# Kernel tuning notes

Hardware: AMD Instinct MI355X
Metric: run time of the kernel (lower is better)

## Reference

```python
import jax, jax.numpy as jnp
import numpy as np

N_NODES = 100000
N_EDGES = 1000000
C_IN, C_HID, C_OUT = 128, 64, 32


def _gcn_layer(x, W, b, src, dst, n):
    """PyG GCNConv with default add_self_loops=True, symmetric normalization.

    x: [N, in], W: [in, out], b: [out], src/dst: [E] int
    """
    h = x @ W  # [N, out] -- transform before aggregation
    # degree of each node counting the added self loop
    deg = jax.ops.segment_sum(jnp.ones_like(dst, dtype=h.dtype), dst, num_segments=n) + 1.0
    dinv = jax.lax.rsqrt(deg)  # deg >= 1 so always finite
    norm = dinv[src] * dinv[dst]  # [E]
    msg = h[src] * norm[:, None]  # [E, out]
    agg = jax.ops.segment_sum(msg, dst, num_segments=n)  # [N, out]
    # self-loop contribution: norm_ii = dinv_i * dinv_i
    out = agg + h * (dinv * dinv)[:, None]
    return out + b


def setup_inputs() -> dict:
    key = jax.random.key(0)
    k1, k2, k3, k4 = jax.random.split(key, 4)
    x = jax.random.normal(k1, (N_NODES, C_IN), dtype=jnp.float32)
    edge_index = jax.random.randint(k2, (2, N_EDGES), 0, N_NODES, dtype=jnp.int64)
    # Glorot-style init for the two GCN layers
    W1 = jax.random.normal(k3, (C_IN, C_HID), dtype=jnp.float32) / np.sqrt(C_IN)
    b1 = jnp.zeros((C_HID,), dtype=jnp.float32)
    W2 = jax.random.normal(k4, (C_HID, C_OUT), dtype=jnp.float32) / np.sqrt(C_HID)
    b2 = jnp.zeros((C_OUT,), dtype=jnp.float32)
    return {"x": x, "edge_index": edge_index, "W1": W1, "b1": b1, "W2": W2, "b2": b2}


def reference(x, edge_index, W1, b1, W2, b2):
    src, dst = edge_index[0], edge_index[1]
    n = x.shape[0]
    h = _gcn_layer(x, W1, b1, src, dst, n)
    h = jax.nn.relu(h)  # Dropout(0.1) is identity in eval mode
    out = _gcn_layer(h, W2, b2, src, dst, n)
    return out
```

## Files before the change

kernel.cpp:

```cpp
#include <hip/hip_runtime.h>
#include <hip/hip_fp16.h>

#define N_NODES 100000
#define N_EDGES 1000000
#define C_IN 128
#define C_HID 64
#define C_OUT 32
#define NB1 ((N_NODES + 255) / 256)
#define GT_BLOCKS 1563
#define RG_RANK_BLOCKS 781
#define RG_GRID 2344
#define AGG1_BLOCKS 6250

__global__ __launch_bounds__(256) void k_rg1(const unsigned int* __restrict__ ei,
                                             int* __restrict__ deg,
                                             int* __restrict__ rank,
                                             const float* __restrict__ x,
                                             const float* __restrict__ W1,
                                             __half* __restrict__ hs1h) {
    __shared__ float xt[64 * C_IN];
    const int bid = blockIdx.x;
    const int m = bid % 3;
    const int r = bid / 3;

    if (m == 2) {
        const bool is64 = __all(ei[2 * (threadIdx.x & 63) + 1] == 0u);
        const int T = RG_RANK_BLOCKS * 256;
        const int t = r * 256 + threadIdx.x;
        int d[6];
#pragma unroll
        for (int i = 0; i < 6; ++i) {
            int e = t + i * T;
            if (e < N_EDGES)
                d[i] = is64 ? ((const int2*)ei)[(size_t)N_EDGES + e].x
                            : (int)ei[(size_t)N_EDGES + e];
        }
        int rk[6];
#pragma unroll
        for (int i = 0; i < 6; ++i) {
            int e = t + i * T;
            if (e < N_EDGES) rk[i] = atomicAdd(&deg[d[i]], 1);
        }
#pragma unroll
        for (int i = 0; i < 6; ++i) {
            int e = t + i * T;
            if (e < N_EDGES) __builtin_nontemporal_store(rk[i], &rank[e]);
        }
        return;
    }

    const int tile = 2 * r + m;
    if (tile >= GT_BLOCKS) return;
    const int t = threadIdx.x;
    {
        const float4* x4g = (const float4*)x;
        float4* xt4w = (float4*)xt;
        const size_t base = (size_t)tile * 64 * (C_IN / 4);
        const size_t xmax = (size_t)N_NODES * (C_IN / 4) - 1;
#pragma unroll
        for (int j = 0; j < 8; ++j) {
            size_t idx = base + t + j * 256;
            if (idx > xmax) idx = xmax;
            xt4w[t + j * 256] = x4g[idx];
        }
    }
    __syncthreads();
    const int c2 = t & 31;
    const int h  = (t >> 5) & 1;
    const int wid = t >> 6;
    const int lrow0 = wid * 16 + h * 8;
    const int grow0 = tile * 64 + lrow0;
    const float4* xt4 = (const float4*)xt;

    float acc0[8] = {0, 0, 0, 0, 0, 0, 0, 0};
    float acc1[8] = {0, 0, 0, 0, 0, 0, 0, 0};
#pragma unroll 2
    for (int k4 = 0; k4 < C_IN / 4; ++k4) {
        float4 xv[8];
#pragma unroll
        for (int rr = 0; rr < 8; ++rr)
            xv[rr] = xt4[(lrow0 + rr) * (C_IN / 4) + k4];
        float2 wv[4];
#pragma unroll
        for (int j = 0; j < 4; ++j)
            wv[j] = *reinterpret_cast<const float2*>(&W1[(k4 * 4 + j) * C_HID + 2 * c2]);
#pragma unroll
        for (int rr = 0; rr < 8; ++rr) {
            acc0[rr] = fmaf(xv[rr].x, wv[0].x, acc0[rr]);
            acc1[rr] = fmaf(xv[rr].x, wv[0].y, acc1[rr]);
            acc0[rr] = fmaf(xv[rr].y, wv[1].x, acc0[rr]);
            acc1[rr] = fmaf(xv[rr].y, wv[1].y, acc1[rr]);
            acc0[rr] = fmaf(xv[rr].z, wv[2].x, acc0[rr]);
            acc1[rr] = fmaf(xv[rr].z, wv[2].y, acc1[rr]);
            acc0[rr] = fmaf(xv[rr].w, wv[3].x, acc0[rr]);
            acc1[rr] = fmaf(xv[rr].w, wv[3].y, acc1[rr]);
        }
    }
    __half2* h2o = (__half2*)hs1h;
#pragma unroll
    for (int rr = 0; rr < 8; ++rr) {
        int gr = grow0 + rr;
        if (gr < N_NODES)
            h2o[(size_t)gr * 32 + c2] = __floats2half2_rn(acc0[rr], acc1[rr]);
    }
}

__global__ __launch_bounds__(256) void k_scan1(const int* __restrict__ deg,
                                               int* __restrict__ rowstart,
                                               int* __restrict__ blksum,
                                               float* __restrict__ dinv) {
    __shared__ int sm[256];
    int i = blockIdx.x * 256 + threadIdx.x;
    int v = (i < N_NODES) ? deg[i] : 0;
    if (i < N_NODES) dinv[i] = rsqrtf((float)v + 1.0f);
    sm[threadIdx.x] = v;
    __syncthreads();
    for (int o = 1; o < 256; o <<= 1) {
        int t = (threadIdx.x >= o) ? sm[threadIdx.x - o] : 0;
        __syncthreads();
        sm[threadIdx.x] += t;
        __syncthreads();
    }
    if (i < N_NODES) rowstart[i] = sm[threadIdx.x] - v;
    if (threadIdx.x == 255) blksum[blockIdx.x] = sm[255];
}

__global__ __launch_bounds__(512) void k_scan2(const int* __restrict__ blksum,
                                               int* __restrict__ blkoff) {
    __shared__ int sm[512];
    int v = (threadIdx.x < NB1) ? blksum[threadIdx.x] : 0;
    sm[threadIdx.x] = v;
    __syncthreads();
    for (int o = 1; o < 512; o <<= 1) {
        int t = (threadIdx.x >= o) ? sm[threadIdx.x - o] : 0;
        __syncthreads();
        sm[threadIdx.x] += t;
        __syncthreads();
    }
    if (threadIdx.x < NB1) blkoff[threadIdx.x] = sm[threadIdx.x] - v;
}

__global__ __launch_bounds__(256) void k_scan3(int* __restrict__ rowstart,
                                               const int* __restrict__ blkoff) {
    int i = blockIdx.x * 256 + threadIdx.x;
    if (i < N_NODES) rowstart[i] += blkoff[i >> 8];
    if (i == 0) rowstart[N_NODES] = N_EDGES;
}

__global__ __launch_bounds__(256) void k_fill2(const unsigned int* __restrict__ ei,
                                               const int* __restrict__ rowstart,
                                               const int* __restrict__ rank,
                                               int* __restrict__ esrc) {
    const bool is64 = __all(ei[2 * (threadIdx.x & 63) + 1] == 0u);
    const int T = gridDim.x * 256;
    const int t = blockIdx.x * 256 + threadIdx.x;
#pragma unroll
    for (int i = 0; i < 4; ++i) {
        int e = t + i * T;
        if (e < N_EDGES) {
            int s, d;
            if (is64) {
                s = ((const int2*)ei)[e].x;
                d = ((const int2*)ei)[(size_t)N_EDGES + e].x;
            } else {
                s = (int)ei[e];
                d = (int)ei[(size_t)N_EDGES + e];
            }
            int p = rowstart[d] + rank[e];
            __builtin_nontemporal_store(s, &esrc[p]);
        }
    }
}

__global__ __launch_bounds__(256) void k_agg1g2(const int* __restrict__ rowstart,
                                                const int* __restrict__ esrc,
                                                const __half* __restrict__ hs1h,
                                                const float* __restrict__ dinv,
                                                const float* __restrict__ b1,
                                                const float* __restrict__ W2,
                                                __half* __restrict__ hs2h) {
    __shared__ float2 yrow[4][32];
    const int wid = threadIdx.x >> 6;
    const int lane = threadIdx.x & 63;
    const int c2 = lane & 31;
    const int eo = lane >> 5;
    float Wreg[32];
#pragma unroll
    for (int kk = 0; kk < 16; ++kk) {
        Wreg[2 * kk]     = W2[(32 * eo + 2 * kk) * C_OUT + c2];
        Wreg[2 * kk + 1] = W2[(32 * eo + 2 * kk + 1) * C_OUT + c2];
    }
    const __half2* h2 = (const __half2*)hs1h;
    const float2 bb = { b1[2 * c2], b1[2 * c2 + 1] };
    const int waveId = blockIdx.x * 4 + wid;

    for (int node = waveId; node < N_NODES; node += AGG1_BLOCKS * 4) {
        const int beg = rowstart[node], end = rowstart[node + 1];
        float2 acc; acc.x = 0.f; acc.y = 0.f;
        for (int j0 = beg; j0 < end; j0 += 16) {
            const int jj = j0 + eo;
            int idx[8];
#pragma unroll
            for (int s = 0; s < 8; ++s) {
                int j = jj + 2 * s;
                idx[s] = esrc[j < end ? j : beg];
            }
            float ds[8];
#pragma unroll
            for (int s = 0; s < 8; ++s)
                ds[s] = (jj + 2 * s < end) ? dinv[idx[s]] : 0.f;
            float2 v[8];
#pragma unroll
            for (int s = 0; s < 8; ++s)
                v[s] = __half22float2(h2[(size_t)idx[s] * 32 + c2]);
#pragma unroll
            for (int s = 0; s < 8; ++s) {
                acc.x = fmaf(ds[s], v[s].x, acc.x);
                acc.y = fmaf(ds[s], v[s].y, acc.y);
            }
        }
        acc.x += __shfl_xor(acc.x, 32);
        acc.y += __shfl_xor(acc.y, 32);
        const float dv = dinv[node];
        float2 self = __half22float2(h2[(size_t)node * 32 + c2]);
        float2 y;
        y.x = fmaxf(fmaf(dv, fmaf(dv, self.x, acc.x), bb.x), 0.f);
        y.y = fmaxf(fmaf(dv, fmaf(dv, self.y, acc.y), bb.y), 0.f);
        yrow[wid][c2] = y;
        __builtin_amdgcn_wave_barrier();
        float o = 0.f;
#pragma unroll
        for (int kk = 0; kk < 16; ++kk) {
            float2 yv = yrow[wid][16 * eo + kk];
            o = fmaf(yv.x, Wreg[2 * kk], o);
            o = fmaf(yv.y, Wreg[2 * kk + 1], o);
        }
        __builtin_amdgcn_wave_barrier();
        o += __shfl_xor(o, 32);
        if (eo == 0)
            hs2h[(size_t)node * C_OUT + c2] = __float2half(o * dv);
    }
}

__global__ __launch_bounds__(256) void k_agg2(const int* __restrict__ rowstart,
                                              const int* __restrict__ esrc,
                                              const __half* __restrict__ hs2h,
                                              const float* __restrict__ dinv,
                                              const float* __restrict__ b2,
                                              float* __restrict__ out) {
    const int node = blockIdx.x * 4 + (threadIdx.x >> 6);
    const int lane = threadIdx.x & 63;
    const int c2 = lane & 15;
    const int eo = lane >> 4;
    const __half2* h2 = (const __half2*)hs2h;
    const int beg = rowstart[node], end = rowstart[node + 1];
    float2 acc; acc.x = 0.f; acc.y = 0.f;
    for (int j0 = beg; j0 < end; j0 += 16) {
        const int jj = j0 + eo;
        int idx[4];
#pragma unroll
        for (int s = 0; s < 4; ++s) {
            int j = jj + 4 * s;
            idx[s] = esrc[j < end ? j : beg];
        }
        float2 v[4];
#pragma unroll
        for (int s = 0; s < 4; ++s)
            v[s] = __half22float2(h2[(size_t)idx[s] * 16 + c2]);
#pragma unroll
        for (int s = 0; s < 4; ++s) {
            if (jj + 4 * s < end) { acc.x += v[s].x; acc.y += v[s].y; }
        }
    }
    acc.x += __shfl_xor(acc.x, 16);
    acc.y += __shfl_xor(acc.y, 16);
    acc.x += __shfl_xor(acc.x, 32);
    acc.y += __shfl_xor(acc.y, 32);
    if (eo == 0) {
        float2 self = __half22float2(h2[(size_t)node * 16 + c2]);
        float dv = dinv[node];
        float2 o;
        o.x = fmaf(dv, acc.x + self.x, b2[2 * c2]);
        o.y = fmaf(dv, acc.y + self.y, b2[2 * c2 + 1]);
        reinterpret_cast<float2*>(out)[(size_t)node * 16 + c2] = o;
    }
}

extern "C" void kernel_launch(void* const* d_in, const int* in_sizes, int n_in,
                              void* d_out, int out_size, void* d_ws, size_t ws_size,
                              hipStream_t stream) {
    const float* x  = (const float*)d_in[0];
    const unsigned int* ei = (const unsigned int*)d_in[1];
    const float* W1 = (const float*)d_in[2];
    const float* b1 = (const float*)d_in[3];
    const float* W2 = (const float*)d_in[4];
    const float* b2 = (const float*)d_in[5];
    float* out = (float*)d_out;

    char* ws = (char*)d_ws;
    size_t off = 0;
    auto take = [&](size_t bytes) {
        char* p = ws + off;
        off += (bytes + 255) & ~(size_t)255;
        return p;
    };
    int*    esrc     = (int*)   take((size_t)N_EDGES * 4);
    int*    rank     = (int*)   take((size_t)N_EDGES * 4);
    int*    deg      = (int*)   take((size_t)N_NODES * 4);
    int*    rowstart = (int*)   take((size_t)(N_NODES + 1) * 4);
    int*    blksum   = (int*)   take((size_t)NB1 * 4);
    int*    blkoff   = (int*)   take((size_t)NB1 * 4);
    float*  dinv     = (float*) take((size_t)N_NODES * 4);
    __half* hs1h     = (__half*)take((size_t)N_NODES * C_HID * 2);
    __half* hs2h     = (__half*)take((size_t)N_NODES * C_OUT * 2);

    hipMemsetAsync(deg, 0, (size_t)N_NODES * 4, stream);
    k_rg1<<<RG_GRID, 256, 0, stream>>>(ei, deg, rank, x, W1, hs1h);

    k_scan1<<<NB1, 256, 0, stream>>>(deg, rowstart, blksum, dinv);
    k_scan2<<<1, 512, 0, stream>>>(blksum, blkoff);
    k_scan3<<<NB1, 256, 0, stream>>>(rowstart, blkoff);

    k_fill2<<<1024, 256, 0, stream>>>(ei, rowstart, rank, esrc);

    k_agg1g2<<<AGG1_BLOCKS, 256, 0, stream>>>(rowstart, esrc, hs1h, dinv, b1, W2, hs2h);

    k_agg2<<<N_NODES / 4, 256, 0, stream>>>(rowstart, esrc, hs2h, dinv, b2, out);
}
```

Baseline: 272.6 us.

## Merge scan and CSR fill into one persistent kernel with grid barriers

Replaces the three-kernel scan and the separate fill kernel with a single 196-block kernel. It uses atomic-counter grid barriers to sequence the local scan, the block-offset scan, the rowstart write and the esrc scatter. The fill loop is also batched four edges at a time so loads issue before the scatter stores. This removes three kernel launches and their gaps. In exchange it relies on all 196 blocks being co-resident for the spin barriers, and the fill phase runs on fewer threads than before.

Result: slower. 415.0 us (+52.3%).

```diff
diff --git a/kernel.cpp b/kernel.cpp
--- a/kernel.cpp
+++ b/kernel.cpp
@@ -6,11 +6,12 @@
 #define C_IN 128
 #define C_HID 64
 #define C_OUT 32
-#define NB1 ((N_NODES + 255) / 256)
 #define GT_BLOCKS 1563
 #define RG_RANK_BLOCKS 781
 #define RG_GRID 2344
 #define AGG1_BLOCKS 6250
+#define SF_BLOCKS 196
+#define SF_NPB 512
 
 __global__ __launch_bounds__(256) void k_rg1(const unsigned int* __restrict__ ei,
                                              int* __restrict__ deg,
@@ -105,70 +106,87 @@
     }
 }
 
-__global__ __launch_bounds__(256) void k_scan1(const int* __restrict__ deg,
-                                               int* __restrict__ rowstart,
-                                               int* __restrict__ blksum,
-                                               float* __restrict__ dinv) {
-    __shared__ int sm[256];
-    int i = blockIdx.x * 256 + threadIdx.x;
+__device__ __forceinline__ void gbar(int* cnt, int n) {
+    __threadfence();
+    __syncthreads();
+    if (threadIdx.x == 0) {
+        atomicAdd(cnt, 1);
+        while (atomicAdd(cnt, 0) < n) __builtin_amdgcn_s_sleep(1);
+    }
+    __syncthreads();
+    __threadfence();
+}
+
+__global__ __launch_bounds__(512) void k_scanfill(const unsigned int* __restrict__ ei,
+                                                  const int* __restrict__ deg,
+                                                  const int* __restrict__ rank,
+                                                  int* __restrict__ rowstart,
+                                                  float* __restrict__ dinv,
+                                                  int* __restrict__ esrc,
+                                                  int* __restrict__ blksum,
+                                                  int* __restrict__ barcnt) {
+    __shared__ int sm[SF_NPB];
+    const int b = blockIdx.x;
+    const int t = threadIdx.x;
+    const int i = b * SF_NPB + t;
+
     int v = (i < N_NODES) ? deg[i] : 0;
     if (i < N_NODES) dinv[i] = rsqrtf((float)v + 1.0f);
-    sm[threadIdx.x] = v;
+    sm[t] = v;
     __syncthreads();
-    for (int o = 1; o < 256; o <<= 1) {
-        int t = (threadIdx.x >= o) ? sm[threadIdx.x - o] : 0;
+    for (int o = 1; o < SF_NPB; o <<= 1) {
+        int u = (t >= o) ? sm[t - o] : 0;
         __syncthreads();
-        sm[threadIdx.x] += t;
+        sm[t] += u;
         __syncthreads();
     }
-    if (i < N_NODES) rowstart[i] = sm[threadIdx.x] - v;
-    if (threadIdx.x == 255) blksum[blockIdx.x] = sm[255];
-}
-
-__global__ __launch_bounds__(512) void k_scan2(const int* __restrict__ blksum,
-                                               int* __restrict__ blkoff) {
-    __shared__ int sm[512];
-    int v = (threadIdx.x < NB1) ? blksum[threadIdx.x] : 0;
-    sm[threadIdx.x] = v;
-    __syncthreads();
-    for (int o = 1; o < 512; o <<= 1) {
-        int t = (threadIdx.x >= o) ? sm[threadIdx.x - o] : 0;
+    const int local_excl = sm[t] - v;
+    if (t == SF_NPB - 1) blksum[b] = sm[SF_NPB - 1];
+
+    gbar(barcnt + 0, SF_BLOCKS);
+
+    if (b == 0) {
+        int s = (t < SF_BLOCKS) ? blksum[t] : 0;
+        sm[t] = s;
         __syncthreads();
-        sm[threadIdx.x] += t;
-        __syncthreads();
-    }
-    if (threadIdx.x < NB1) blkoff[threadIdx.x] = sm[threadIdx.x] - v;
-}
-
-__global__ __launch_bounds__(256) void k_scan3(int* __restrict__ rowstart,
-                                               const int* __restrict__ blkoff) {
-    int i = blockIdx.x * 256 + threadIdx.x;
-    if (i < N_NODES) rowstart[i] += blkoff[i >> 8];
+        for (int o = 1; o < SF_NPB; o <<= 1) {
+            int u = (t >= o) ? sm[t - o] : 0;
+            __syncthreads();
+            sm[t] += u;
+            __syncthreads();
+        }
+        if (t < SF_BLOCKS) blksum[t] = sm[t] - s;
+    }
+
+    gbar(barcnt + 1, SF_BLOCKS);
+
+    if (i < N_NODES) rowstart[i] = local_excl + blksum[b];
     if (i == 0) rowstart[N_NODES] = N_EDGES;
-}
-
-__global__ __launch_bounds__(256) void k_fill2(const unsigned int* __restrict__ ei,
-                                               const int* __restrict__ rowstart,
-                                               const int* __restrict__ rank,
-                                               int* __restrict__ esrc) {
-    const bool is64 = __all(ei[2 * (threadIdx.x & 63) + 1] == 0u);
-    const int T = gridDim.x * 256;
-    const int t = blockIdx.x * 256 + threadIdx.x;
-#pragma unroll
-    for (int i = 0; i < 4; ++i) {
-        int e = t + i * T;
-        if (e < N_EDGES) {
-            int s, d;
+
+    gbar(barcnt + 2, SF_BLOCKS);
+
+    const bool is64 = __all(ei[2 * (t & 63) + 1] == 0u);
+    const int T = SF_BLOCKS * SF_NPB;
+    for (int base = b * SF_NPB + t; base < N_EDGES; base += 4 * T) {
+        int e[4], s[4], d[4], p[4];
+#pragma unroll
+        for (int k = 0; k < 4; ++k) {
+            e[k] = base + k * T;
+            int ec = (e[k] < N_EDGES) ? e[k] : 0;
             if (is64) {
-                s = ((const int2*)ei)[e].x;
-                d = ((const int2*)ei)[(size_t)N_EDGES + e].x;
+                s[k] = ((const int2*)ei)[ec].x;
+                d[k] = ((const int2*)ei)[(size_t)N_EDGES + ec].x;
             } else {
-                s = (int)ei[e];
-                d = (int)ei[(size_t)N_EDGES + e];
+                s[k] = (int)ei[ec];
+                d[k] = (int)ei[(size_t)N_EDGES + ec];
             }
-            int p = rowstart[d] + rank[e];
-            __builtin_nontemporal_store(s, &esrc[p]);
-        }
+        }
+#pragma unroll
+        for (int k = 0; k < 4; ++k)
+            p[k] = rowstart[d[k]] + rank[(e[k] < N_EDGES) ? e[k] : 0];
+#pragma unroll
+        for (int k = 0; k < 4; ++k)
+            if (e[k] < N_EDGES) __builtin_nontemporal_store(s[k], &esrc[p[k]]);
     }
 }
 
@@ -306,22 +324,21 @@
     };
     int*    esrc     = (int*)   take((size_t)N_EDGES * 4);
     int*    rank     = (int*)   take((size_t)N_EDGES * 4);
-    int*    deg      = (int*)   take((size_t)N_NODES * 4);
+    int*    degz     = (int*)   take((size_t)N_NODES * 4 + 256);
+    int*    deg      = degz;
+    int*    barcnt   = degz + N_NODES;
     int*    rowstart = (int*)   take((size_t)(N_NODES + 1) * 4);
-    int*    blksum   = (int*)   take((size_t)NB1 * 4);
-    int*    blkoff   = (int*)   take((size_t)NB1 * 4);
+    int*    blksum   = (int*)   take(256 * 4);
     float*  dinv     = (float*) take((size_t)N_NODES * 4);
     __half* hs1h     = (__half*)take((size_t)N_NODES * C_HID * 2);
     __half* hs2h     = (__half*)take((size_t)N_NODES * C_OUT * 2);
 
-    hipMemsetAsync(deg, 0, (size_t)N_NODES * 4, stream);
+    hipMemsetAsync(degz, 0, (size_t)N_NODES * 4 + 256, stream);
+
     k_rg1<<<RG_GRID, 256, 0, stream>>>(ei, deg, rank, x, W1, hs1h);
 
-    k_scan1<<<NB1, 256, 0, stream>>>(deg, rowstart, blksum, dinv);
-    k_scan2<<<1, 512, 0, stream>>>(blksum, blkoff);
-    k_scan3<<<NB1, 256, 0, stream>>>(rowstart, blkoff);
-
-    k_fill2<<<1024, 256, 0, stream>>>(ei, rowstart, rank, esrc);
+    k_scanfill<<<SF_BLOCKS, 512, 0, stream>>>(ei, deg, rank, rowstart, dinv,
+                                              esrc, blksum, barcnt);
 
     k_agg1g2<<<AGG1_BLOCKS, 256, 0, stream>>>(rowstart, esrc, hs1h, dinv, b1, W2, hs2h);
 
```

## Replace three-kernel degree scan with single-block wavefront scan kernel

Applied to the files above, without the earlier changes.

Replaces the three-pass exclusive scan (per-block scan, block-sum scan, offset add) with one kernel launched as a single 1024-thread block. Each wavefront reduces a contiguous chunk of degrees, the wave totals are scanned serially in shared memory, then each wave does a shuffle-based inclusive scan over its chunk while writing rowstart and dinv. This removes two kernel launches and the intermediate blksum/blkoff arrays. In exchange, the scan now runs on one CU and reads deg twice, with a serial 98-step loop per wave, so it gives up the grid-wide parallelism of the old version.

Measured after the change: 313.1 us. +14.9%, slower.

```diff
diff --git a/kernel.cpp b/kernel.cpp
--- a/kernel.cpp
+++ b/kernel.cpp
@@ -6,7 +6,6 @@
 #define C_IN 128
 #define C_HID 64
 #define C_OUT 32
-#define NB1 ((N_NODES + 255) / 256)
 #define GT_BLOCKS 1563
 #define RG_RANK_BLOCKS 781
 #define RG_GRID 2344
@@ -105,46 +104,46 @@
     }
 }
 
-__global__ __launch_bounds__(256) void k_scan1(const int* __restrict__ deg,
-                                               int* __restrict__ rowstart,
-                                               int* __restrict__ blksum,
-                                               float* __restrict__ dinv) {
-    __shared__ int sm[256];
-    int i = blockIdx.x * 256 + threadIdx.x;
-    int v = (i < N_NODES) ? deg[i] : 0;
-    if (i < N_NODES) dinv[i] = rsqrtf((float)v + 1.0f);
-    sm[threadIdx.x] = v;
+__global__ __launch_bounds__(1024) void k_scanone(const int* __restrict__ deg,
+                                                  int* __restrict__ rowstart,
+                                                  float* __restrict__ dinv) {
+    __shared__ int wsum[16];
+    const int t = threadIdx.x;
+    const int lane = t & 63;
+    const int w = t >> 6;
+    const int base = w * 6272;
+    int s = 0;
+    for (int k = 0; k < 98; ++k) {
+        int i = base + k * 64 + lane;
+        s += (i < N_NODES) ? deg[i] : 0;
+    }
+#pragma unroll
+    for (int o = 1; o < 64; o <<= 1) s += __shfl_xor(s, o);
+    if (lane == 0) wsum[w] = s;
     __syncthreads();
-    for (int o = 1; o < 256; o <<= 1) {
-        int t = (threadIdx.x >= o) ? sm[threadIdx.x - o] : 0;
-        __syncthreads();
-        sm[threadIdx.x] += t;
-        __syncthreads();
-    }
-    if (i < N_NODES) rowstart[i] = sm[threadIdx.x] - v;
-    if (threadIdx.x == 255) blksum[blockIdx.x] = sm[255];
-}
-
-__global__ __launch_bounds__(512) void k_scan2(const int* __restrict__ blksum,
-                                               int* __restrict__ blkoff) {
-    __shared__ int sm[512];
-    int v = (threadIdx.x < NB1) ? blksum[threadIdx.x] : 0;
-    sm[threadIdx.x] = v;
+    if (t == 0) {
+        int run = 0;
+#pragma unroll
+        for (int k = 0; k < 16; ++k) { int v = wsum[k]; wsum[k] = run; run += v; }
+    }
     __syncthreads();
-    for (int o = 1; o < 512; o <<= 1) {
-        int t = (threadIdx.x >= o) ? sm[threadIdx.x - o] : 0;
-        __syncthreads();
-        sm[threadIdx.x] += t;
-        __syncthreads();
-    }
-    if (threadIdx.x < NB1) blkoff[threadIdx.x] = sm[threadIdx.x] - v;
-}
-
-__global__ __launch_bounds__(256) void k_scan3(int* __restrict__ rowstart,
-                                               const int* __restrict__ blkoff) {
-    int i = blockIdx.x * 256 + threadIdx.x;
-    if (i < N_NODES) rowstart[i] += blkoff[i >> 8];
-    if (i == 0) rowstart[N_NODES] = N_EDGES;
+    int rowoff = wsum[w];
+    for (int k = 0; k < 98; ++k) {
+        int i = base + k * 64 + lane;
+        int v = (i < N_NODES) ? deg[i] : 0;
+        int incl = v;
+#pragma unroll
+        for (int o = 1; o < 64; o <<= 1) {
+            int y = __shfl_up(incl, o);
+            if (lane >= o) incl += y;
+        }
+        if (i < N_NODES) {
+            rowstart[i] = rowoff + incl - v;
+            dinv[i] = rsqrtf((float)v + 1.0f);
+        }
+        rowoff += __shfl(incl, 63);
+    }
+    if (t == 0) rowstart[N_NODES] = N_EDGES;
 }
 
 __global__ __launch_bounds__(256) void k_fill2(const unsigned int* __restrict__ ei,
@@ -308,18 +307,15 @@
     int*    rank     = (int*)   take((size_t)N_EDGES * 4);
     int*    deg      = (int*)   take((size_t)N_NODES * 4);
     int*    rowstart = (int*)   take((size_t)(N_NODES + 1) * 4);
-    int*    blksum   = (int*)   take((size_t)NB1 * 4);
-    int*    blkoff   = (int*)   take((size_t)NB1 * 4);
     float*  dinv     = (float*) take((size_t)N_NODES * 4);
     __half* hs1h     = (__half*)take((size_t)N_NODES * C_HID * 2);
     __half* hs2h     = (__half*)take((size_t)N_NODES * C_OUT * 2);
 
     hipMemsetAsync(deg, 0, (size_t)N_NODES * 4, stream);
+
     k_rg1<<<RG_GRID, 256, 0, stream>>>(ei, deg, rank, x, W1, hs1h);
 
-    k_scan1<<<NB1, 256, 0, stream>>>(deg, rowstart, blksum, dinv);
-    k_scan2<<<1, 512, 0, stream>>>(blksum, blkoff);
-    k_scan3<<<NB1, 256, 0, stream>>>(rowstart, blkoff);
+    k_scanone<<<1, 1024, 0, stream>>>(deg, rowstart, dinv);
 
     k_fill2<<<1024, 256, 0, stream>>>(ei, rowstart, rank, esrc);
 
```
